# Performance work log

Measured on AMD Instinct MI355X. Metric: run time of the kernel, lower is better.

The kernel has to match this reference:

```python
import jax, jax.numpy as jnp
import numpy as np

NUM_ITERATIONS = 10


def _nearest_neighbor(src, tgt):
    # src: [B,N,3], tgt: [B,M,3] -> indices [B,N] of nearest tgt point per src point
    inner = -2.0 * jnp.einsum('bnd,bmd->bnm', src, tgt)            # [B,N,M]
    xx = jnp.sum(src * src, axis=2, keepdims=True)                  # [B,N,1]
    yy = jnp.sum(tgt * tgt, axis=2, keepdims=True).transpose(0, 2, 1)  # [B,1,M]
    distances = xx + inner + yy                                     # [B,N,M]
    return jnp.argmin(distances, axis=2)                            # [B,N]


def _compute_transformation(src, tgt):
    # src, tgt: [B,N,3] matched pairs -> rigid (R [B,3,3], t [B,3])
    N = src.shape[1]
    c_src = jnp.mean(src, axis=1, keepdims=True)                    # [B,1,3]
    c_tgt = jnp.mean(tgt, axis=1, keepdims=True)                    # [B,1,3]
    H = jnp.einsum('bnd,bne->bde', src - c_src, tgt - c_tgt) / N    # [B,3,3]
    U, S, Vh = jnp.linalg.svd(H, full_matrices=False)
    V = jnp.swapaxes(Vh, -1, -2)                                    # matches torch.svd's V
    R = V @ jnp.swapaxes(U, -1, -2)
    det = jnp.linalg.det(R)                                         # [B]
    sign = 1.0 - 2.0 * (det < 0).astype(src.dtype)                  # +1 or -1
    # torch code scales V[:, :, 2] (third column of V)
    V = V * jnp.concatenate([jnp.ones_like(sign)[:, None],
                             jnp.ones_like(sign)[:, None],
                             sign[:, None]], axis=1)[:, None, :]    # scale col 2
    R = V @ jnp.swapaxes(U, -1, -2)                                 # [B,3,3]
    t = c_tgt[:, 0, :] - jnp.einsum('bij,bj->bi', R, c_src[:, 0, :])  # [B,3]
    return R, t


def _icp(src, tgt):
    transformed_src = src
    R = None
    t = None
    for _ in range(NUM_ITERATIONS):
        indices = _nearest_neighbor(transformed_src, tgt)           # [B,N]
        matched_tgt = jnp.take_along_axis(tgt, indices[:, :, None], axis=1)  # [B,N,3]
        R, t = _compute_transformation(transformed_src, matched_tgt)
        # faithful to torch: x @ R + t (R applied on the right)
        transformed_src = jnp.einsum('bnd,bde->bne', transformed_src, R) + t[:, None, :]
    return R, t, transformed_src


def setup_inputs() -> dict:
    key = jax.random.key(0)
    k1, k2 = jax.random.split(key)
    src = jax.random.normal(k1, (4, 4096, 3), dtype=jnp.float32)
    tgt = jax.random.normal(k2, (4, 4096, 3), dtype=jnp.float32)
    return {"src": src, "tgt": tgt}


def reference(src, tgt):
    # Returns (est_R [B,3,3], est_t [B,3], transformed_source [B,N,3])
    return _icp(src, tgt)
```

## Files before the change

### kernel.cpp

```cpp
#include <hip/hip_runtime.h>
#include <math.h>

#define NB 4
#define NP 4096
#define MP 4096

typedef __bf16 bf16x8 __attribute__((ext_vector_type(8)));
typedef float  f32x16 __attribute__((ext_vector_type(16)));

static __device__ __forceinline__ unsigned short bh(float f) {
    unsigned u = __float_as_uint(f);
    unsigned r = (u + 0x7FFFu + ((u >> 16) & 1u)) >> 16;
    return (unsigned short)r;
}
static __device__ __forceinline__ float hf(unsigned short h) {
    return __uint_as_float(((unsigned)h) << 16);
}

__device__ __forceinline__ void kabsch_f32(const float* s, float* RtL) {
    const float invN = 1.0f / (float)NP;
    float cs[3] = { s[0] * invN, s[1] * invN, s[2] * invN };
    float ct[3] = { s[3] * invN, s[4] * invN, s[5] * invN };
    float H[3][3];
    for (int d = 0; d < 3; ++d)
        for (int e = 0; e < 3; ++e)
            H[d][e] = s[6 + d * 3 + e] * invN - cs[d] * ct[e];

    float A[3][3];
    for (int i = 0; i < 3; ++i)
        for (int j = 0; j < 3; ++j)
            A[i][j] = H[0][i] * H[0][j] + H[1][i] * H[1][j] + H[2][i] * H[2][j];

    float V[3][3] = {{1, 0, 0}, {0, 1, 0}, {0, 0, 1}};
    for (int sweep = 0; sweep < 8; ++sweep) {
        float off = A[0][1] * A[0][1] + A[0][2] * A[0][2] + A[1][2] * A[1][2];
        if (off < 1e-16f) break;
        for (int pi = 0; pi < 3; ++pi) {
            const int p = (pi == 2) ? 1 : 0;
            const int q = (pi == 0) ? 1 : 2;
            float apq = A[p][q];
            if (fabsf(apq) < 1e-30f) continue;
            float theta = (A[q][q] - A[p][p]) / (2.0f * apq);
            float t = 1.0f / (fabsf(theta) + sqrtf(1.0f + theta * theta));
            if (theta < 0.0f) t = -t;
            float cth = 1.0f / sqrtf(1.0f + t * t);
            float sth = t * cth;
            float App = A[p][p], Aqq = A[q][q];
            A[p][p] = App - t * apq;
            A[q][q] = Aqq + t * apq;
            A[p][q] = A[q][p] = 0.0f;
            const int r = 3 - p - q;
            float Apr = A[p][r], Aqr = A[q][r];
            A[p][r] = A[r][p] = cth * Apr - sth * Aqr;
            A[q][r] = A[r][q] = sth * Apr + cth * Aqr;
            for (int i = 0; i < 3; ++i) {
                float Vip = V[i][p], Viq = V[i][q];
                V[i][p] = cth * Vip - sth * Viq;
                V[i][q] = sth * Vip + cth * Viq;
            }
        }
    }
    float lam[3] = { A[0][0], A[1][1], A[2][2] };
    for (int i = 0; i < 2; ++i)
        for (int j = i + 1; j < 3; ++j)
            if (lam[j] > lam[i]) {
                float tl = lam[i]; lam[i] = lam[j]; lam[j] = tl;
                for (int k = 0; k < 3; ++k) {
                    float tv = V[k][i]; V[k][i] = V[k][j]; V[k][j] = tv;
                }
            }

    float U[3][3];
    for (int k = 0; k < 3; ++k) {
        float w0 = H[0][0] * V[0][k] + H[0][1] * V[1][k] + H[0][2] * V[2][k];
        float w1 = H[1][0] * V[0][k] + H[1][1] * V[1][k] + H[1][2] * V[2][k];
        float w2 = H[2][0] * V[0][k] + H[2][1] * V[1][k] + H[2][2] * V[2][k];
        float nrm = sqrtf(w0 * w0 + w1 * w1 + w2 * w2);
        if (nrm > 1e-20f) {
            U[0][k] = w0 / nrm; U[1][k] = w1 / nrm; U[2][k] = w2 / nrm;
        } else {
            U[0][k] = U[1][0] * U[2][1] - U[2][0] * U[1][1];
            U[1][k] = U[2][0] * U[0][1] - U[0][0] * U[2][1];
            U[2][k] = U[0][0] * U[1][1] - U[1][0] * U[0][1];
        }
    }

    float detH = H[0][0] * (H[1][1] * H[2][2] - H[1][2] * H[2][1])
               - H[0][1] * (H[1][0] * H[2][2] - H[1][2] * H[2][0])
               + H[0][2] * (H[1][0] * H[2][1] - H[1][1] * H[2][0]);
    float sgn = (detH < 0.0f) ? -1.0f : 1.0f;

    float R[3][3];
    for (int i = 0; i < 3; ++i)
        for (int j = 0; j < 3; ++j)
            R[i][j] = V[i][0] * U[j][0] + V[i][1] * U[j][1] + sgn * V[i][2] * U[j][2];
    float tv[3];
    for (int i = 0; i < 3; ++i)
        tv[i] = ct[i] - (R[i][0] * cs[0] + R[i][1] * cs[1] + R[i][2] * cs[2]);

    for (int i = 0; i < 3; ++i)
        for (int j = 0; j < 3; ++j)
            RtL[i * 3 + j] = R[i][j];
    for (int i = 0; i < 3; ++i) RtL[9 + i] = tv[i];
}

__global__ __launch_bounds__(256) void icp_init(const float* __restrict__ tgt,
                                                float4* __restrict__ tgt4,
                                                uint4* __restrict__ Bbuf) {
    const int t    = blockIdx.x * 256 + threadIdx.x;
    const int b    = t >> 13;
    const int rem  = t & 8191;
    const int tile = rem >> 6;
    const int lane = rem & 63;
    const int n    = lane & 31;
    const int h    = lane >> 5;
    const int gt   = b * MP + tile * 32 + n;

    float x = tgt[gt * 3 + 0];
    float y = tgt[gt * 3 + 1];
    float z = tgt[gt * 3 + 2];
    float wv = x * x + y * y + z * z;

    unsigned short xh = bh(x), xl = bh(x - hf(xh));
    unsigned short yh = bh(y), yl = bh(y - hf(yh));
    unsigned short zh = bh(z), zl = bh(z - hf(zh));
    unsigned short wh = bh(wv), wl = bh(wv - hf(wh));
    const unsigned short ONE = 0x3F80;

    unsigned short s0, s1, s2, s3, s4, s5, s6, s7;
    if (h == 0) { s0 = xh; s1 = xh; s2 = xl; s3 = xl;
                  s4 = yh; s5 = yh; s6 = yl; s7 = yl; }
    else        { s0 = zh; s1 = zh; s2 = zl; s3 = zl;
                  s4 = wh; s5 = wl; s6 = ONE; s7 = ONE; }
    uint4 u;
    u.x = (unsigned)s0 | ((unsigned)s1 << 16);
    u.y = (unsigned)s2 | ((unsigned)s3 << 16);
    u.z = (unsigned)s4 | ((unsigned)s5 << 16);
    u.w = (unsigned)s6 | ((unsigned)s7 << 16);
    Bbuf[t] = u;

    if (h == 0) tgt4[gt] = make_float4(x, y, z, wv);
}

__global__ __launch_bounds__(1024, 4) void icp_scan(
        const float* __restrict__ src,
        const float4* __restrict__ tgt4,
        const uint4* __restrict__ Bbuf,
        float* __restrict__ S,
        const float* __restrict__ pprev,
        float* __restrict__ pout,
        int first) {
    __shared__ unsigned CK[512];
    __shared__ float RtL[12];

    const int blk = blockIdx.x;
    const int b   = blk >> 6;
    const int g   = blk & 63;
    const int tid = threadIdx.x;
    const int w   = tid >> 6;
    const int l   = tid & 63;
    const int ts  = w & 1;
    const int tr  = w >> 1;
    const int gsrc = b * NP + g * 64 + l;

    const uint4* Bw = Bbuf + (b * 128 + tr * 16) * 64;
    uint4 fb[4];
    fb[0] = Bw[l];
    fb[1] = Bw[64 + l];
    fb[2] = Bw[128 + l];
    fb[3] = Bw[192 + l];

    const float* P = first ? src : S;
    float x0 = P[gsrc * 3 + 0];
    float y0 = P[gsrc * 3 + 1];
    float z0 = P[gsrc * 3 + 2];

    if (w == 0) {
        if (first) {
            if (l < 12) RtL[l] = (l == 0 || l == 4 || l == 8) ? 1.0f : 0.0f;
        } else {
            const float4* rp = (const float4*)(pprev + (b * 64 + l) * 16);
            float4 r0 = rp[0], r1 = rp[1], r2 = rp[2], r3 = rp[3];
            float sm[15] = { r0.x, r0.y, r0.z, r0.w, r1.x, r1.y, r1.z, r1.w,
                             r2.x, r2.y, r2.z, r2.w, r3.x, r3.y, r3.z };
            #pragma unroll
            for (int k = 0; k < 15; ++k) {
                float v = sm[k];
                v += __shfl_down(v, 32);
                v += __shfl_down(v, 16);
                v += __shfl_down(v, 8);
                v += __shfl_down(v, 4);
                v += __shfl_down(v, 2);
                v += __shfl_down(v, 1);
                sm[k] = v;
            }
            if (l == 0) kabsch_f32(sm, RtL);
        }
    }
    __syncthreads();

    float px = x0 * RtL[0] + y0 * RtL[3] + z0 * RtL[6] + RtL[9];
    float py = x0 * RtL[1] + y0 * RtL[4] + z0 * RtL[7] + RtL[10];
    float pz = x0 * RtL[2] + y0 * RtL[5] + z0 * RtL[8] + RtL[11];
    if (w == 1) {
        S[gsrc * 3 + 0] = px;
        S[gsrc * 3 + 1] = py;
        S[gsrc * 3 + 2] = pz;
    }

    const int h = l >> 5;
    union { unsigned short s[8]; bf16x8 v; } Af;
    {
        const int j3 = ts * 32 + (l & 31);
        float pxj = __shfl(px, j3);
        float pyj = __shfl(py, j3);
        float pzj = __shfl(pz, j3);
        float ax = -2.0f * pxj, ay = -2.0f * pyj, az = -2.0f * pzj;
        float qv = pxj * pxj + pyj * pyj + pzj * pzj + 1.0f;
        unsigned short axh = bh(ax), axl = bh(ax - hf(axh));
        unsigned short ayh = bh(ay), ayl = bh(ay - hf(ayh));
        unsigned short azh = bh(az), azl = bh(az - hf(azh));
        unsigned short qh  = bh(qv), ql  = bh(qv - hf(qh));
        const unsigned short ONE = 0x3F80;
        if (h == 0) {
            Af.s[0] = axh; Af.s[1] = axl; Af.s[2] = axh; Af.s[3] = axl;
            Af.s[4] = ayh; Af.s[5] = ayl; Af.s[6] = ayh; Af.s[7] = ayl;
        } else {
            Af.s[0] = azh; Af.s[1] = azl; Af.s[2] = azh; Af.s[3] = azl;
            Af.s[4] = ONE; Af.s[5] = ONE; Af.s[6] = qh;  Af.s[7] = ql;
        }
    }

    f32x16 zero;
    #pragma unroll
    for (int i = 0; i < 16; ++i) zero[i] = 0.0f;

    float best[16];
    #pragma unroll
    for (int r = 0; r < 16; ++r) best[r] = __uint_as_float(0x7F7FFFFFu);

    const int col = l & 31;

    #pragma unroll
    for (int t = 0; t < 16; ++t) {
        bf16x8 Bf = __builtin_bit_cast(bf16x8, fb[t & 3]);
        if (t < 12) fb[t & 3] = Bw[(t + 4) * 64 + l];
        f32x16 d16 = __builtin_amdgcn_mfma_f32_32x32x16_bf16(Af.v, Bf, zero,
                                                             0, 0, 0);
        const unsigned idxk = (unsigned)((tr * 16 + t) * 32 + col);
        #pragma unroll
        for (int r = 0; r < 16; ++r) {
            float key = __uint_as_float(
                (__float_as_uint(d16[r]) & 0xFFFFF000u) | idxk);
            best[r] = fminf(best[r], key);
        }
    }

    #pragma unroll
    for (int r = 0; r < 16; ++r) {
        float v = best[r];
        v = fminf(v, __shfl_xor(v, 1));
        v = fminf(v, __shfl_xor(v, 2));
        v = fminf(v, __shfl_xor(v, 4));
        v = fminf(v, __shfl_xor(v, 8));
        v = fminf(v, __shfl_xor(v, 16));
        best[r] = v;
    }
    if ((l & 31) == 0) {
        #pragma unroll
        for (int r = 0; r < 16; ++r) {
            const int row = (r & 3) + 8 * (r >> 2) + 4 * h;
            CK[tr * 64 + ts * 32 + row] = __float_as_uint(best[r]);
        }
    }
    __syncthreads();

    if (w == 0) {
        unsigned kb = CK[l];
        #pragma unroll
        for (int k = 1; k < 8; ++k) {
            unsigned kk = CK[k * 64 + l];
            kb = kk < kb ? kk : kb;
        }
        const int idx = kb & 0xFFF;
        float4 mt = tgt4[b * MP + idx];
        const float tx = mt.x, ty = mt.y, tz = mt.z;

        float v[15];
        v[0]  = px;      v[1]  = py;      v[2]  = pz;
        v[3]  = tx;      v[4]  = ty;      v[5]  = tz;
        v[6]  = px * tx; v[7]  = px * ty; v[8]  = px * tz;
        v[9]  = py * tx; v[10] = py * ty; v[11] = py * tz;
        v[12] = pz * tx; v[13] = pz * ty; v[14] = pz * tz;
        #pragma unroll
        for (int k = 0; k < 15; ++k) {
            float s = v[k];
            s += __shfl_down(s, 32);
            s += __shfl_down(s, 16);
            s += __shfl_down(s, 8);
            s += __shfl_down(s, 4);
            s += __shfl_down(s, 2);
            s += __shfl_down(s, 1);
            v[k] = s;
        }
        if (l == 0) {
            float* pp = pout + blk * 16;
            #pragma unroll
            for (int k = 0; k < 15; ++k) pp[k] = v[k];
        }
    }
}

__global__ __launch_bounds__(256) void icp_final(
        const float* __restrict__ S,
        const float* __restrict__ plast,
        float* __restrict__ out) {
    __shared__ float RtL[12];
    const int bk  = blockIdx.x;
    const int tid = threadIdx.x;
    const int gid = bk * 256 + tid;
    const int b   = gid >> 12;

    if (tid < 64) {
        const float4* rp = (const float4*)(plast + (b * 64 + tid) * 16);
        float4 r0 = rp[0], r1 = rp[1], r2 = rp[2], r3 = rp[3];
        float sm[15] = { r0.x, r0.y, r0.z, r0.w, r1.x, r1.y, r1.z, r1.w,
                         r2.x, r2.y, r2.z, r2.w, r3.x, r3.y, r3.z };
        #pragma unroll
        for (int k = 0; k < 15; ++k) {
            float v = sm[k];
            v += __shfl_down(v, 32);
            v += __shfl_down(v, 16);
            v += __shfl_down(v, 8);
            v += __shfl_down(v, 4);
            v += __shfl_down(v, 2);
            v += __shfl_down(v, 1);
            sm[k] = v;
        }
        if (tid == 0) kabsch_f32(sm, RtL);
    }
    __syncthreads();

    float x = S[gid * 3 + 0];
    float y = S[gid * 3 + 1];
    float z = S[gid * 3 + 2];
    out[48 + gid * 3 + 0] = x * RtL[0] + y * RtL[3] + z * RtL[6] + RtL[9];
    out[48 + gid * 3 + 1] = x * RtL[1] + y * RtL[4] + z * RtL[7] + RtL[10];
    out[48 + gid * 3 + 2] = x * RtL[2] + y * RtL[5] + z * RtL[8] + RtL[11];
    if ((bk & 15) == 0) {
        if (tid < 9) out[b * 9 + tid] = RtL[tid];
        if (tid < 3) out[36 + b * 3 + tid] = RtL[9 + tid];
    }
}

extern "C" void kernel_launch(void* const* d_in, const int* in_sizes, int n_in,
                              void* d_out, int out_size, void* d_ws, size_t ws_size,
                              hipStream_t stream) {
    const float* src = (const float*)d_in[0];
    const float* tgt = (const float*)d_in[1];
    float* out = (float*)d_out;

    float* W     = (float*)d_ws;
    float4* tgt4 = (float4*)W;
    uint4*  Bbuf = (uint4*)(W + 65536);
    float*  S    = W + 65536 + 131072;
    float*  pA   = S + 49152;
    float*  pB   = pA + 4096;
    float* bufs[2] = { pA, pB };

    icp_init<<<128, 256, 0, stream>>>(tgt, tgt4, Bbuf);
    for (int k = 0; k < 10; ++k) {
        icp_scan<<<256, 1024, 0, stream>>>(src, tgt4, Bbuf, S,
                                           bufs[(k + 1) & 1], bufs[k & 1],
                                           k == 0 ? 1 : 0);
    }
    icp_final<<<64, 256, 0, stream>>>(S, bufs[1], out);
}
```

Before: 193.8 us.

## Compute Kabsch once per batch in last-arriving block instead of every block

Each scan block used to reload the 64 partial sums of the previous iteration, reduce them and run the serial Kabsch/SVD before doing any work. Now each block publishes its partials, bumps a per-batch arrival counter, and only the last block for a batch reduces and solves. It writes R,t to a workspace that the next launch and the final kernel read directly. This takes the redundant serial SVD off the start of every block. In exchange it adds atomics, relies on relaxed ordering plus an explicit waitcnt for visibility, and uses a separate counter and partial slot per iteration.

```diff
diff --git a/kernel.cpp b/kernel.cpp
--- a/kernel.cpp
+++ b/kernel.cpp
@@ -106,8 +106,16 @@
 
 __global__ __launch_bounds__(256) void icp_init(const float* __restrict__ tgt,
                                                 float4* __restrict__ tgt4,
-                                                uint4* __restrict__ Bbuf) {
+                                                uint4* __restrict__ Bbuf,
+                                                unsigned* __restrict__ arr,
+                                                float* __restrict__ RtLws) {
     const int t    = blockIdx.x * 256 + threadIdx.x;
+    if (t < 40) arr[t] = 0;
+    if (t < 48) {
+        const int j = t % 12;
+        RtLws[t] = (j == 0 || j == 4 || j == 8) ? 1.0f : 0.0f;
+    }
+
     const int b    = t >> 13;
     const int rem  = t & 8191;
     const int tile = rem >> 6;
@@ -143,13 +151,13 @@
 }
 
 __global__ __launch_bounds__(1024, 4) void icp_scan(
-        const float* __restrict__ src,
+        const float* __restrict__ Pin,
         const float4* __restrict__ tgt4,
         const uint4* __restrict__ Bbuf,
         float* __restrict__ S,
-        const float* __restrict__ pprev,
-        float* __restrict__ pout,
-        int first) {
+        float* __restrict__ RtLws,
+        float* __restrict__ pslot,
+        unsigned* __restrict__ arr) {
     __shared__ unsigned CK[512];
     __shared__ float RtL[12];
 
@@ -170,33 +178,11 @@
     fb[2] = Bw[128 + l];
     fb[3] = Bw[192 + l];
 
-    const float* P = first ? src : S;
-    float x0 = P[gsrc * 3 + 0];
-    float y0 = P[gsrc * 3 + 1];
-    float z0 = P[gsrc * 3 + 2];
-
-    if (w == 0) {
-        if (first) {
-            if (l < 12) RtL[l] = (l == 0 || l == 4 || l == 8) ? 1.0f : 0.0f;
-        } else {
-            const float4* rp = (const float4*)(pprev + (b * 64 + l) * 16);
-            float4 r0 = rp[0], r1 = rp[1], r2 = rp[2], r3 = rp[3];
-            float sm[15] = { r0.x, r0.y, r0.z, r0.w, r1.x, r1.y, r1.z, r1.w,
-                             r2.x, r2.y, r2.z, r2.w, r3.x, r3.y, r3.z };
-            #pragma unroll
-            for (int k = 0; k < 15; ++k) {
-                float v = sm[k];
-                v += __shfl_down(v, 32);
-                v += __shfl_down(v, 16);
-                v += __shfl_down(v, 8);
-                v += __shfl_down(v, 4);
-                v += __shfl_down(v, 2);
-                v += __shfl_down(v, 1);
-                sm[k] = v;
-            }
-            if (l == 0) kabsch_f32(sm, RtL);
-        }
-    }
+    float x0 = Pin[gsrc * 3 + 0];
+    float y0 = Pin[gsrc * 3 + 1];
+    float z0 = Pin[gsrc * 3 + 2];
+
+    if (w == 0 && l < 12) RtL[l] = RtLws[b * 12 + l];
     __syncthreads();
 
     float px = x0 * RtL[0] + y0 * RtL[3] + z0 * RtL[6] + RtL[9];
@@ -303,17 +289,53 @@
             s += __shfl_down(s, 1);
             v[k] = s;
         }
+
+        int isLast = 0;
         if (l == 0) {
-            float* pp = pout + blk * 16;
+            float* pp = pslot + blk * 16;
             #pragma unroll
-            for (int k = 0; k < 15; ++k) pp[k] = v[k];
+            for (int k = 0; k < 15; ++k)
+                __hip_atomic_store(&pp[k], v[k], __ATOMIC_RELAXED,
+                                   __HIP_MEMORY_SCOPE_AGENT);
+            asm volatile("s_waitcnt vmcnt(0)" ::: "memory");
+            unsigned prev = __hip_atomic_fetch_add(&arr[b], 1u,
+                                                   __ATOMIC_RELAXED,
+                                                   __HIP_MEMORY_SCOPE_AGENT);
+            isLast = (prev == 63u);
+        }
+        isLast = __shfl(isLast, 0);
+
+        if (isLast) {
+            const float* rp = pslot + (b * 64 + l) * 16;
+            float sm[15];
+            #pragma unroll
+            for (int q = 0; q < 15; ++q)
+                sm[q] = __hip_atomic_load(rp + q, __ATOMIC_RELAXED,
+                                          __HIP_MEMORY_SCOPE_AGENT);
+            #pragma unroll
+            for (int q = 0; q < 15; ++q) {
+                float s = sm[q];
+                s += __shfl_down(s, 32);
+                s += __shfl_down(s, 16);
+                s += __shfl_down(s, 8);
+                s += __shfl_down(s, 4);
+                s += __shfl_down(s, 2);
+                s += __shfl_down(s, 1);
+                sm[q] = s;
+            }
+            if (l == 0) {
+                float Rt[12];
+                kabsch_f32(sm, Rt);
+                #pragma unroll
+                for (int j = 0; j < 12; ++j) RtLws[b * 12 + j] = Rt[j];
+            }
         }
     }
 }
 
 __global__ __launch_bounds__(256) void icp_final(
         const float* __restrict__ S,
-        const float* __restrict__ plast,
+        const float* __restrict__ RtLws,
         float* __restrict__ out) {
     __shared__ float RtL[12];
     const int bk  = blockIdx.x;
@@ -321,24 +343,7 @@
     const int gid = bk * 256 + tid;
     const int b   = gid >> 12;
 
-    if (tid < 64) {
-        const float4* rp = (const float4*)(plast + (b * 64 + tid) * 16);
-        float4 r0 = rp[0], r1 = rp[1], r2 = rp[2], r3 = rp[3];
-        float sm[15] = { r0.x, r0.y, r0.z, r0.w, r1.x, r1.y, r1.z, r1.w,
-                         r2.x, r2.y, r2.z, r2.w, r3.x, r3.y, r3.z };
-        #pragma unroll
-        for (int k = 0; k < 15; ++k) {
-            float v = sm[k];
-            v += __shfl_down(v, 32);
-            v += __shfl_down(v, 16);
-            v += __shfl_down(v, 8);
-            v += __shfl_down(v, 4);
-            v += __shfl_down(v, 2);
-            v += __shfl_down(v, 1);
-            sm[k] = v;
-        }
-        if (tid == 0) kabsch_f32(sm, RtL);
-    }
+    if (tid < 12) RtL[tid] = RtLws[b * 12 + tid];
     __syncthreads();
 
     float x = S[gid * 3 + 0];
@@ -360,19 +365,19 @@
     const float* tgt = (const float*)d_in[1];
     float* out = (float*)d_out;
 
-    float* W     = (float*)d_ws;
-    float4* tgt4 = (float4*)W;
-    uint4*  Bbuf = (uint4*)(W + 65536);
-    float*  S    = W + 65536 + 131072;
-    float*  pA   = S + 49152;
-    float*  pB   = pA + 4096;
-    float* bufs[2] = { pA, pB };
-
-    icp_init<<<128, 256, 0, stream>>>(tgt, tgt4, Bbuf);
+    float* W        = (float*)d_ws;
+    float4* tgt4    = (float4*)W;
+    uint4*  Bbuf    = (uint4*)(W + 65536);
+    float*  S       = W + 65536 + 131072;
+    float*  pbuf    = S + 49152;
+    float*  RtLws   = pbuf + 40960;
+    unsigned* arr   = (unsigned*)(RtLws + 48);
+
+    icp_init<<<128, 256, 0, stream>>>(tgt, tgt4, Bbuf, arr, RtLws);
     for (int k = 0; k < 10; ++k) {
-        icp_scan<<<256, 1024, 0, stream>>>(src, tgt4, Bbuf, S,
-                                           bufs[(k + 1) & 1], bufs[k & 1],
-                                           k == 0 ? 1 : 0);
-    }
-    icp_final<<<64, 256, 0, stream>>>(S, bufs[1], out);
-}
+        icp_scan<<<256, 1024, 0, stream>>>(k == 0 ? src : S, tgt4, Bbuf, S,
+                                           RtLws, pbuf + k * 256 * 16,
+                                           arr + k * 4);
+    }
+    icp_final<<<64, 256, 0, stream>>>(S, RtLws, out);
+}
```

Measured after the change: 236.5 us. 22.1% more time.
